# Performance work log

Hardware: AMD Instinct MI355X
Metric: run time of the kernel (lower is better)

Reference implementation:

```python
import jax, jax.numpy as jnp
from jax import lax
import numpy as np

HIDDEN = 1024
GRID = 512
KSIZE = 3
SIGMA = 1.0


def setup_inputs() -> dict:
    key = jax.random.key(0)
    ks = jax.random.split(key, 10)
    B, E, D = 4, 256, 128
    s = 1.0 / np.sqrt(HIDDEN)
    sf = 1.0 / np.sqrt(2 * GRID)
    return {
        "encoder_hidden": jax.random.normal(ks[0], (B, E, HIDDEN), jnp.float32),
        "decoder_hidden": jax.random.normal(ks[1], (B, D, HIDDEN), jnp.float32),
        "encoder_mask": jnp.ones((B, E), jnp.float32),
        "decoder_mask": jnp.ones((B, D), jnp.float32),
        "W_enc": jax.random.uniform(ks[2], (GRID, HIDDEN), jnp.float32, -s, s),
        "b_enc": jax.random.uniform(ks[3], (GRID,), jnp.float32, -s, s),
        "W_dec": jax.random.uniform(ks[4], (GRID, HIDDEN), jnp.float32, -s, s),
        "b_dec": jax.random.uniform(ks[5], (GRID,), jnp.float32, -s, s),
        "W_fus": jax.random.uniform(ks[6], (GRID, 2 * GRID), jnp.float32, -sf, sf),
        "b_fus": jax.random.uniform(ks[7], (GRID,), jnp.float32, -sf, sf),
    }


def _gauss_kernel():
    coords = jnp.arange(KSIZE, dtype=jnp.float32) - KSIZE // 2
    g = jnp.exp(-coords ** 2 / (2.0 * SIGMA ** 2))
    return g / g.sum()


def _blur_axis(x, axis, k):
    # zero-padded 'same' 1D conv with kernel size 3 along `axis`
    pad = [(0, 0)] * x.ndim
    pad[axis] = (1, 1)
    xp = jnp.pad(x, pad)
    n = x.shape[axis]
    return (k[0] * lax.slice_in_dim(xp, 0, n, axis=axis)
            + k[1] * lax.slice_in_dim(xp, 1, n + 1, axis=axis)
            + k[2] * lax.slice_in_dim(xp, 2, n + 2, axis=axis))


def reference(encoder_hidden, decoder_hidden, encoder_mask, decoder_mask,
              W_enc, b_enc, W_dec, b_dec, W_fus, b_fus):
    # projections, masked
    enc_proj = (jnp.einsum('beh,gh->beg', encoder_hidden, W_enc) + b_enc) * encoder_mask[..., None]
    dec_proj = (jnp.einsum('bdh,gh->bdg', decoder_hidden, W_dec) + b_dec) * decoder_mask[..., None]
    # fusion Linear over concat([enc, dec]) == W_fus[:, :G] @ enc + W_fus[:, G:] @ dec + b
    Wf_e = W_fus[:, :GRID]
    Wf_d = W_fus[:, GRID:]
    enc_term = jnp.einsum('beg,og->beo', enc_proj, Wf_e)   # [B,E,G]
    dec_term = jnp.einsum('bdg,og->bdo', dec_proj, Wf_d)   # [B,D,G]
    grid = dec_term[:, :, None, :] + enc_term[:, None, :, :] + b_fus  # [B,D,E,G]
    # separable depthwise Gaussian blur: enc axis (2) then dec axis (1)
    k = _gauss_kernel()
    blurred = _blur_axis(grid, 2, k)
    blurred = _blur_axis(blurred, 1, k)
    # binary mask via L2 norm threshold (threshold=0.0)
    mask = (jnp.linalg.norm(blurred, axis=-1) > 0.0).astype(jnp.float32)
    return (grid, mask)
```

## Files before the change

### kernel.cpp

```cpp
#include <hip/hip_runtime.h>

namespace {

constexpr int kGrid = 512;
constexpr int kB = 4;
constexpr int kE = 256;
constexpr int kD = 128;

constexpr float kG0   = 0.27406862f;
constexpr float kG1   = 0.45186276f;
constexpr float kEdge = kG0 + kG1;

typedef __attribute__((ext_vector_type(8))) short bf16x8;
typedef __attribute__((ext_vector_type(4))) float f32x4;

__device__ __forceinline__ ushort f2bf(float f) {
  union { float f; uint u; } v{f};
  return (ushort)((v.u + 0x7fffu + ((v.u >> 16) & 1u)) >> 16);
}

__global__ __launch_bounds__(256)
void convert_all(const float* __restrict__ enc_h, const float* __restrict__ dec_h,
                 const float* __restrict__ W_fus, ushort* __restrict__ hid,
                 ushort* __restrict__ wfus) {
  const int idx = (blockIdx.x * 256 + threadIdx.x) * 4;
  const float* src; ushort* dst;
  if (idx < 1048576)       { src = enc_h + idx;             dst = hid + idx; }
  else if (idx < 1572864)  { src = dec_h + (idx - 1048576); dst = hid + idx; }
  else                     { src = W_fus + (idx - 1572864); dst = wfus + (idx - 1572864); }
  const float4 v = *(const float4*)src;
  ushort4 o; o.x = f2bf(v.x); o.y = f2bf(v.y); o.z = f2bf(v.z); o.w = f2bf(v.w);
  *(ushort4*)dst = o;
}

__global__ __launch_bounds__(256)
void transpose_cvt(const float* __restrict__ W_enc, const float* __restrict__ W_dec,
                   ushort* __restrict__ WT) {
  const float* Wsrc = blockIdx.z ? W_dec : W_enc;
  ushort* outT = WT + (size_t)blockIdx.z * 1024 * 512;
  __shared__ ushort Ts[32][36];
  const int h0 = blockIdx.x * 32, g0 = blockIdx.y * 32;
  const int tx = threadIdx.x & 7, ty = threadIdx.x >> 3;
  const float4 v = *(const float4*)(Wsrc + (size_t)(g0 + ty) * 1024 + h0 + tx * 4);
  Ts[tx * 4 + 0][ty] = f2bf(v.x); Ts[tx * 4 + 1][ty] = f2bf(v.y);
  Ts[tx * 4 + 2][ty] = f2bf(v.z); Ts[tx * 4 + 3][ty] = f2bf(v.w);
  __syncthreads();
  ushort4 o; o.x = Ts[ty][tx * 4 + 0]; o.y = Ts[ty][tx * 4 + 1];
  o.z = Ts[ty][tx * 4 + 2]; o.w = Ts[ty][tx * 4 + 3];
  *(ushort4*)(outT + (size_t)(h0 + ty) * 512 + g0 + tx * 4) = o;
}

__global__ __launch_bounds__(256)
void cvec_kernel(const float* __restrict__ W_fus, const float* __restrict__ b_enc,
                 const float* __restrict__ b_dec, float* __restrict__ cvec) {
  const int wid = blockIdx.x * 4 + (threadIdx.x >> 6);
  const int lane = threadIdx.x & 63;
  const int sel = wid >> 9, o = wid & 511;
  const float* wrow = W_fus + (size_t)o * 1024 + sel * 512 + lane * 8;
  const float* bv = (sel ? b_dec : b_enc) + lane * 8;
  float s = 0.f;
#pragma unroll
  for (int j = 0; j < 8; ++j) s += wrow[j] * bv[j];
#pragma unroll
  for (int off = 32; off; off >>= 1) s += __shfl_down(s, off);
  if (!lane) cvec[wid] = s;
}


__global__ __launch_bounds__(256)
void gemm_w(const ushort* __restrict__ wfus, const ushort* __restrict__ WT,
            ushort* __restrict__ Mmat) {
  const int z = blockIdx.z;
  const short* A = (const short*)wfus + z * 512;
  const short* B = (const short*)WT + (size_t)z * 1024 * 512;
  ushort* Cw = Mmat + (size_t)z * 512 * 1024;
  __shared__ short As[64][72], Bs[64][72];
  const int tid = threadIdx.x, wid = tid >> 6, lane = tid & 63;
  const int row0 = blockIdx.y * 64, col0 = blockIdx.x * 64;
  const int srow = tid >> 2, sc = tid & 3;
  const short* Ap = A + (size_t)(row0 + srow) * 1024 + sc * 8;
  const short* Bp = B + (size_t)(col0 + srow) * 512 + sc * 8;
  const int wr = (wid >> 1) * 32, wc = (wid & 1) * 32;
  const int r16 = lane & 15, kb = lane >> 4;
  f32x4 acc[2][2] = {};
  for (int k0 = 0; k0 < 512; k0 += 64) {
    const bf16x8 alo = *(const bf16x8*)(Ap + k0);
    const bf16x8 ahi = *(const bf16x8*)(Ap + k0 + 32);
    const bf16x8 blo = *(const bf16x8*)(Bp + k0);
    const bf16x8 bhi = *(const bf16x8*)(Bp + k0 + 32);
    __syncthreads();
    *(bf16x8*)&As[srow][sc * 8] = alo;  *(bf16x8*)&As[srow][(sc + 4) * 8] = ahi;
    *(bf16x8*)&Bs[srow][sc * 8] = blo;  *(bf16x8*)&Bs[srow][(sc + 4) * 8] = bhi;
    __syncthreads();
#pragma unroll
    for (int ks = 0; ks < 2; ++ks) {
      const int ko = ks * 32 + kb * 8;
      const bf16x8 a0 = *(const bf16x8*)&As[wr + r16][ko];
      const bf16x8 a1 = *(const bf16x8*)&As[wr + 16 + r16][ko];
      const bf16x8 b0 = *(const bf16x8*)&Bs[wc + r16][ko];
      const bf16x8 b1 = *(const bf16x8*)&Bs[wc + 16 + r16][ko];
      acc[0][0] = __builtin_amdgcn_mfma_f32_16x16x32_bf16(a0, b0, acc[0][0], 0, 0, 0);
      acc[0][1] = __builtin_amdgcn_mfma_f32_16x16x32_bf16(a0, b1, acc[0][1], 0, 0, 0);
      acc[1][0] = __builtin_amdgcn_mfma_f32_16x16x32_bf16(a1, b0, acc[1][0], 0, 0, 0);
      acc[1][1] = __builtin_amdgcn_mfma_f32_16x16x32_bf16(a1, b1, acc[1][1], 0, 0, 0);
    }
  }
#pragma unroll
  for (int i = 0; i < 2; ++i)
#pragma unroll
    for (int j = 0; j < 2; ++j)
#pragma unroll
      for (int q = 0; q < 4; ++q) {
        const int r = row0 + wr + i * 16 + kb * 4 + q;
        const int c = col0 + wc + j * 16 + r16;
        Cw[(size_t)r * 1024 + c] = f2bf(acc[i][j][q]);
      }
}

__global__ __launch_bounds__(256)
void gemm_t(const ushort* __restrict__ hid, const ushort* __restrict__ Mmat,
            const float* __restrict__ cvec, const float* __restrict__ enc_mask,
            const float* __restrict__ dec_mask, float* __restrict__ term) {
  const int row0 = blockIdx.y * 64, col0 = blockIdx.x * 64;
  const bool enc = row0 < 1024;
  const short* A = (const short*)hid;
  const short* B = (const short*)Mmat + (enc ? 0 : (size_t)512 * 1024);
  const float* cv = cvec + (enc ? 0 : 512);
  const float* rmb = enc ? enc_mask : (dec_mask - 1024);
  __shared__ short As[64][72], Bs[64][72];
  const int tid = threadIdx.x, wid = tid >> 6, lane = tid & 63;
  const int srow = tid >> 2, sc = tid & 3;
  const short* Ap = A + (size_t)(row0 + srow) * 1024 + sc * 8;
  const short* Bp = B + (size_t)(col0 + srow) * 1024 + sc * 8;
  const int wr = (wid >> 1) * 32, wc = (wid & 1) * 32;
  const int r16 = lane & 15, kb = lane >> 4;
  f32x4 acc[2][2] = {};
  for (int k0 = 0; k0 < 1024; k0 += 64) {
    const bf16x8 alo = *(const bf16x8*)(Ap + k0);
    const bf16x8 ahi = *(const bf16x8*)(Ap + k0 + 32);
    const bf16x8 blo = *(const bf16x8*)(Bp + k0);
    const bf16x8 bhi = *(const bf16x8*)(Bp + k0 + 32);
    __syncthreads();
    *(bf16x8*)&As[srow][sc * 8] = alo;  *(bf16x8*)&As[srow][(sc + 4) * 8] = ahi;
    *(bf16x8*)&Bs[srow][sc * 8] = blo;  *(bf16x8*)&Bs[srow][(sc + 4) * 8] = bhi;
    __syncthreads();
#pragma unroll
    for (int ks = 0; ks < 2; ++ks) {
      const int ko = ks * 32 + kb * 8;
      const bf16x8 a0 = *(const bf16x8*)&As[wr + r16][ko];
      const bf16x8 a1 = *(const bf16x8*)&As[wr + 16 + r16][ko];
      const bf16x8 b0 = *(const bf16x8*)&Bs[wc + r16][ko];
      const bf16x8 b1 = *(const bf16x8*)&Bs[wc + 16 + r16][ko];
      acc[0][0] = __builtin_amdgcn_mfma_f32_16x16x32_bf16(a0, b0, acc[0][0], 0, 0, 0);
      acc[0][1] = __builtin_amdgcn_mfma_f32_16x16x32_bf16(a0, b1, acc[0][1], 0, 0, 0);
      acc[1][0] = __builtin_amdgcn_mfma_f32_16x16x32_bf16(a1, b0, acc[1][0], 0, 0, 0);
      acc[1][1] = __builtin_amdgcn_mfma_f32_16x16x32_bf16(a1, b1, acc[1][1], 0, 0, 0);
    }
  }
#pragma unroll
  for (int i = 0; i < 2; ++i)
#pragma unroll
    for (int j = 0; j < 2; ++j)
#pragma unroll
      for (int q = 0; q < 4; ++q) {
        const int r = row0 + wr + i * 16 + kb * 4 + q;
        const int c = col0 + wc + j * 16 + r16;
        term[(size_t)r * 512 + c] = (acc[i][j][q] + cv[c]) * rmb[r];
      }
}

__global__ __launch_bounds__(256)
void assemble(const float* __restrict__ dec_term, const float* __restrict__ enc_term,
              const float* __restrict__ b_fus, float* __restrict__ out) {
  const int bd = blockIdx.x;
  const int b  = bd >> 7;
  const int ebase = blockIdx.y * 64;
  const int tid = threadIdx.x;
  const int eo = tid >> 7;
  const int o4 = (tid & 127) << 2;
  const float4 dv = *(const float4*)(dec_term + (size_t)bd * kGrid + o4);
  const float4 bv = *(const float4*)(b_fus + o4);
  const float4 db = make_float4(dv.x + bv.x, dv.y + bv.y, dv.z + bv.z, dv.w + bv.w);
  const float* encb = enc_term + (size_t)b * kE * kGrid;
  float* outb = out + (size_t)bd * kE * kGrid;
#pragma unroll 4
  for (int e0 = 0; e0 < 64; e0 += 2) {
    const int e = ebase + e0 + eo;
    const float4 ev = *(const float4*)(encb + (size_t)e * kGrid + o4);
    *(float4*)(outb + (size_t)e * kGrid + o4) =
        make_float4(db.x + ev.x, db.y + ev.y, db.z + ev.z, db.w + ev.w);
  }
}

__global__ __launch_bounds__(256)
void blur_both(const float* __restrict__ dec_term, const float* __restrict__ enc_term,
               float* __restrict__ dec_blur, float* __restrict__ enc_blur) {
  const int idx = blockIdx.x * 256 + threadIdx.x;
  constexpr int decN = kB * kD * kGrid;
  if (idx < decN) {
    const int d = (idx >> 9) & (kD - 1);
    float v = kG1 * dec_term[idx];
    if (d > 0)      v += kG0 * dec_term[idx - kGrid];
    if (d < kD - 1) v += kG0 * dec_term[idx + kGrid];
    dec_blur[idx] = v;
  } else {
    const int j = idx - decN;
    if (j < kB * kE * kGrid) {
      const int e = (j >> 9) & (kE - 1);
      float v = kG1 * enc_term[j];
      if (e > 0)      v += kG0 * enc_term[j - kGrid];
      if (e < kE - 1) v += kG0 * enc_term[j + kGrid];
      enc_blur[j] = v;
    }
  }
}

__global__ __launch_bounds__(256)
void mask_kernel(const float* __restrict__ dec_blur, const float* __restrict__ enc_blur,
                 const float* __restrict__ b_fus, float* __restrict__ mask_out) {
  const int bid = blockIdx.x * 4 + (threadIdx.x >> 6);
  const int e = bid & (kE - 1);
  const int d = (bid >> 8) & (kD - 1);
  const int b = bid >> 15;
  const float sE  = (e == 0 || e == kE - 1) ? kEdge : 1.f;
  const float sD  = (d == 0 || d == kD - 1) ? kEdge : 1.f;
  const float sED = sE * sD;
  const int lane = threadIdx.x & 63;
  const float* dp = dec_blur + ((size_t)(b * kD + d)) * kGrid + lane * 8;
  const float* ep = enc_blur + ((size_t)(b * kE + e)) * kGrid + lane * 8;
  const float* zp = b_fus + lane * 8;
  float acc = 0.f;
#pragma unroll
  for (int j = 0; j < 2; ++j) {
    const float4 dv = *(const float4*)(dp + 4 * j);
    const float4 ev = *(const float4*)(ep + 4 * j);
    const float4 zv = *(const float4*)(zp + 4 * j);
    float t;
    t = dv.x * sE + ev.x * sD + zv.x * sED; acc += t * t;
    t = dv.y * sE + ev.y * sD + zv.y * sED; acc += t * t;
    t = dv.z * sE + ev.z * sD + zv.z * sED; acc += t * t;
    t = dv.w * sE + ev.w * sD + zv.w * sED; acc += t * t;
  }
#pragma unroll
  for (int off = 32; off; off >>= 1) acc += __shfl_down(acc, off);
  if (!lane) mask_out[bid] = (acc > 0.f) ? 1.f : 0.f;
}

}

extern "C" void kernel_launch(void* const* d_in, const int* in_sizes, int n_in,
                              void* d_out, int out_size, void* d_ws, size_t ws_size,
                              hipStream_t stream) {
  const float* enc_h  = (const float*)d_in[0];
  const float* dec_h  = (const float*)d_in[1];
  const float* enc_m  = (const float*)d_in[2];
  const float* dec_m  = (const float*)d_in[3];
  const float* W_enc  = (const float*)d_in[4];
  const float* b_enc  = (const float*)d_in[5];
  const float* W_dec  = (const float*)d_in[6];
  const float* b_dec  = (const float*)d_in[7];
  const float* W_fus  = (const float*)d_in[8];
  const float* b_fus  = (const float*)d_in[9];
  float* out = (float*)d_out;
  float* ws  = (float*)d_ws;

  float* term = ws;
  float* cvec = ws + 786432;
  ushort* hid  = (ushort*)(ws + 787456);
  ushort* wfus = hid + 1572864;
  ushort* WT   = wfus + 524288;
  ushort* Mmat = WT + 1048576;
  float* enc_term = term;
  float* dec_term = term + 524288;
  float* dec_blur = (float*)hid;
  float* enc_blur = dec_blur + 262144;

  const dim3 blk(256);
  hipLaunchKernelGGL(convert_all, dim3(2048), blk, 0, stream, enc_h, dec_h, W_fus, hid, wfus);
  hipLaunchKernelGGL(transpose_cvt, dim3(32, 16, 2), blk, 0, stream, W_enc, W_dec, WT);
  hipLaunchKernelGGL(cvec_kernel, dim3(256), blk, 0, stream, W_fus, b_enc, b_dec, cvec);
  hipLaunchKernelGGL(gemm_w, dim3(16, 8, 2), blk, 0, stream, wfus, WT, Mmat);
  hipLaunchKernelGGL(gemm_t, dim3(8, 24), blk, 0, stream, hid, Mmat, cvec, enc_m, dec_m, term);
  hipLaunchKernelGGL(assemble, dim3(kB * kD, kE / 64), blk, 0, stream,
                     dec_term, enc_term, b_fus, out);
  hipLaunchKernelGGL(blur_both, dim3(3072), blk, 0, stream,
                     dec_term, enc_term, dec_blur, enc_blur);
  hipLaunchKernelGGL(mask_kernel, dim3(kB * kD * kE / 4), blk, 0, stream,
                     dec_blur, enc_blur, b_fus, out + (size_t)kB * kD * kE * kGrid);
}
```

Measured before the change: 385.5 us.

## Fuse whole pipeline into one persistent cooperative kernel with grid syncs

Replaces the eight separate kernels with a single cooperative kernel that runs the projection GEMM, the fusion GEMM, the blur, the grid assembly and the mask in phases separated by grid-wide syncs. fp32 inputs are converted to bf16 while being staged into shared memory, which removes the separate conversion and transpose passes. The precomputed combined weight matrix is dropped in favour of computing the projections first and then the fusion GEMM. This cuts launch overhead and intermediate traffic, at the cost of grid synchronisation and of GEMM phases that use only a fraction of the resident blocks.

```diff
diff --git a/kernel.cpp b/kernel.cpp
--- a/kernel.cpp
+++ b/kernel.cpp
@@ -1,11 +1,9 @@
 #include <hip/hip_runtime.h>
+#include <hip/hip_cooperative_groups.h>
+
+namespace cg = cooperative_groups;
 
 namespace {
-
-constexpr int kGrid = 512;
-constexpr int kB = 4;
-constexpr int kE = 256;
-constexpr int kD = 128;
 
 constexpr float kG0   = 0.27406862f;
 constexpr float kG1   = 0.45186276f;
@@ -19,231 +17,208 @@
   return (ushort)((v.u + 0x7fffu + ((v.u >> 16) & 1u)) >> 16);
 }
 
-__global__ __launch_bounds__(256)
-void convert_all(const float* __restrict__ enc_h, const float* __restrict__ dec_h,
-                 const float* __restrict__ W_fus, ushort* __restrict__ hid,
-                 ushort* __restrict__ wfus) {
-  const int idx = (blockIdx.x * 256 + threadIdx.x) * 4;
-  const float* src; ushort* dst;
-  if (idx < 1048576)       { src = enc_h + idx;             dst = hid + idx; }
-  else if (idx < 1572864)  { src = dec_h + (idx - 1048576); dst = hid + idx; }
-  else                     { src = W_fus + (idx - 1572864); dst = wfus + (idx - 1572864); }
-  const float4 v = *(const float4*)src;
-  ushort4 o; o.x = f2bf(v.x); o.y = f2bf(v.y); o.z = f2bf(v.z); o.w = f2bf(v.w);
-  *(ushort4*)dst = o;
-}
-
-__global__ __launch_bounds__(256)
-void transpose_cvt(const float* __restrict__ W_enc, const float* __restrict__ W_dec,
-                   ushort* __restrict__ WT) {
-  const float* Wsrc = blockIdx.z ? W_dec : W_enc;
-  ushort* outT = WT + (size_t)blockIdx.z * 1024 * 512;
-  __shared__ ushort Ts[32][36];
-  const int h0 = blockIdx.x * 32, g0 = blockIdx.y * 32;
-  const int tx = threadIdx.x & 7, ty = threadIdx.x >> 3;
-  const float4 v = *(const float4*)(Wsrc + (size_t)(g0 + ty) * 1024 + h0 + tx * 4);
-  Ts[tx * 4 + 0][ty] = f2bf(v.x); Ts[tx * 4 + 1][ty] = f2bf(v.y);
-  Ts[tx * 4 + 2][ty] = f2bf(v.z); Ts[tx * 4 + 3][ty] = f2bf(v.w);
-  __syncthreads();
-  ushort4 o; o.x = Ts[ty][tx * 4 + 0]; o.y = Ts[ty][tx * 4 + 1];
-  o.z = Ts[ty][tx * 4 + 2]; o.w = Ts[ty][tx * 4 + 3];
-  *(ushort4*)(outT + (size_t)(h0 + ty) * 512 + g0 + tx * 4) = o;
-}
-
-__global__ __launch_bounds__(256)
-void cvec_kernel(const float* __restrict__ W_fus, const float* __restrict__ b_enc,
-                 const float* __restrict__ b_dec, float* __restrict__ cvec) {
-  const int wid = blockIdx.x * 4 + (threadIdx.x >> 6);
-  const int lane = threadIdx.x & 63;
-  const int sel = wid >> 9, o = wid & 511;
-  const float* wrow = W_fus + (size_t)o * 1024 + sel * 512 + lane * 8;
-  const float* bv = (sel ? b_dec : b_enc) + lane * 8;
-  float s = 0.f;
-#pragma unroll
-  for (int j = 0; j < 8; ++j) s += wrow[j] * bv[j];
-#pragma unroll
-  for (int off = 32; off; off >>= 1) s += __shfl_down(s, off);
-  if (!lane) cvec[wid] = s;
-}
-
-
-__global__ __launch_bounds__(256)
-void gemm_w(const ushort* __restrict__ wfus, const ushort* __restrict__ WT,
-            ushort* __restrict__ Mmat) {
-  const int z = blockIdx.z;
-  const short* A = (const short*)wfus + z * 512;
-  const short* B = (const short*)WT + (size_t)z * 1024 * 512;
-  ushort* Cw = Mmat + (size_t)z * 512 * 1024;
+__device__ __forceinline__ void cvt_store16(const float4 v0, const float4 v1,
+                                            const float4 v2, const float4 v3,
+                                            short* dst) {
+  bf16x8 lo, hi;
+  lo[0] = (short)f2bf(v0.x); lo[1] = (short)f2bf(v0.y);
+  lo[2] = (short)f2bf(v0.z); lo[3] = (short)f2bf(v0.w);
+  lo[4] = (short)f2bf(v1.x); lo[5] = (short)f2bf(v1.y);
+  lo[6] = (short)f2bf(v1.z); lo[7] = (short)f2bf(v1.w);
+  hi[0] = (short)f2bf(v2.x); hi[1] = (short)f2bf(v2.y);
+  hi[2] = (short)f2bf(v2.z); hi[3] = (short)f2bf(v2.w);
+  hi[4] = (short)f2bf(v3.x); hi[5] = (short)f2bf(v3.y);
+  hi[6] = (short)f2bf(v3.z); hi[7] = (short)f2bf(v3.w);
+  *(bf16x8*)dst = lo;
+  *(bf16x8*)(dst + 8) = hi;
+}
+
+__global__ __launch_bounds__(256, 3)
+void fused(const float* __restrict__ enc_h, const float* __restrict__ dec_h,
+           const float* __restrict__ enc_m, const float* __restrict__ dec_m,
+           const float* __restrict__ W_enc, const float* __restrict__ b_enc,
+           const float* __restrict__ W_dec, const float* __restrict__ b_dec,
+           const float* __restrict__ W_fus, const float* __restrict__ b_fus,
+           float* __restrict__ out, ushort* __restrict__ proj,
+           float* __restrict__ term, float* __restrict__ dec_blur,
+           float* __restrict__ enc_blur) {
+  cg::grid_group grid = cg::this_grid();
   __shared__ short As[64][72], Bs[64][72];
-  const int tid = threadIdx.x, wid = tid >> 6, lane = tid & 63;
-  const int row0 = blockIdx.y * 64, col0 = blockIdx.x * 64;
+  const int tid = threadIdx.x;
+  const int wid = tid >> 6, lane = tid & 63;
   const int srow = tid >> 2, sc = tid & 3;
-  const short* Ap = A + (size_t)(row0 + srow) * 1024 + sc * 8;
-  const short* Bp = B + (size_t)(col0 + srow) * 512 + sc * 8;
   const int wr = (wid >> 1) * 32, wc = (wid & 1) * 32;
   const int r16 = lane & 15, kb = lane >> 4;
-  f32x4 acc[2][2] = {};
-  for (int k0 = 0; k0 < 512; k0 += 64) {
-    const bf16x8 alo = *(const bf16x8*)(Ap + k0);
-    const bf16x8 ahi = *(const bf16x8*)(Ap + k0 + 32);
-    const bf16x8 blo = *(const bf16x8*)(Bp + k0);
-    const bf16x8 bhi = *(const bf16x8*)(Bp + k0 + 32);
-    __syncthreads();
-    *(bf16x8*)&As[srow][sc * 8] = alo;  *(bf16x8*)&As[srow][(sc + 4) * 8] = ahi;
-    *(bf16x8*)&Bs[srow][sc * 8] = blo;  *(bf16x8*)&Bs[srow][(sc + 4) * 8] = bhi;
-    __syncthreads();
-#pragma unroll
-    for (int ks = 0; ks < 2; ++ks) {
-      const int ko = ks * 32 + kb * 8;
-      const bf16x8 a0 = *(const bf16x8*)&As[wr + r16][ko];
-      const bf16x8 a1 = *(const bf16x8*)&As[wr + 16 + r16][ko];
-      const bf16x8 b0 = *(const bf16x8*)&Bs[wc + r16][ko];
-      const bf16x8 b1 = *(const bf16x8*)&Bs[wc + 16 + r16][ko];
-      acc[0][0] = __builtin_amdgcn_mfma_f32_16x16x32_bf16(a0, b0, acc[0][0], 0, 0, 0);
-      acc[0][1] = __builtin_amdgcn_mfma_f32_16x16x32_bf16(a0, b1, acc[0][1], 0, 0, 0);
-      acc[1][0] = __builtin_amdgcn_mfma_f32_16x16x32_bf16(a1, b0, acc[1][0], 0, 0, 0);
-      acc[1][1] = __builtin_amdgcn_mfma_f32_16x16x32_bf16(a1, b1, acc[1][1], 0, 0, 0);
-    }
-  }
-#pragma unroll
-  for (int i = 0; i < 2; ++i)
-#pragma unroll
-    for (int j = 0; j < 2; ++j)
-#pragma unroll
-      for (int q = 0; q < 4; ++q) {
-        const int r = row0 + wr + i * 16 + kb * 4 + q;
-        const int c = col0 + wc + j * 16 + r16;
-        Cw[(size_t)r * 1024 + c] = f2bf(acc[i][j][q]);
-      }
-}
-
-__global__ __launch_bounds__(256)
-void gemm_t(const ushort* __restrict__ hid, const ushort* __restrict__ Mmat,
-            const float* __restrict__ cvec, const float* __restrict__ enc_mask,
-            const float* __restrict__ dec_mask, float* __restrict__ term) {
-  const int row0 = blockIdx.y * 64, col0 = blockIdx.x * 64;
-  const bool enc = row0 < 1024;
-  const short* A = (const short*)hid;
-  const short* B = (const short*)Mmat + (enc ? 0 : (size_t)512 * 1024);
-  const float* cv = cvec + (enc ? 0 : 512);
-  const float* rmb = enc ? enc_mask : (dec_mask - 1024);
-  __shared__ short As[64][72], Bs[64][72];
-  const int tid = threadIdx.x, wid = tid >> 6, lane = tid & 63;
-  const int srow = tid >> 2, sc = tid & 3;
-  const short* Ap = A + (size_t)(row0 + srow) * 1024 + sc * 8;
-  const short* Bp = B + (size_t)(col0 + srow) * 1024 + sc * 8;
-  const int wr = (wid >> 1) * 32, wc = (wid & 1) * 32;
-  const int r16 = lane & 15, kb = lane >> 4;
-  f32x4 acc[2][2] = {};
-  for (int k0 = 0; k0 < 1024; k0 += 64) {
-    const bf16x8 alo = *(const bf16x8*)(Ap + k0);
-    const bf16x8 ahi = *(const bf16x8*)(Ap + k0 + 32);
-    const bf16x8 blo = *(const bf16x8*)(Bp + k0);
-    const bf16x8 bhi = *(const bf16x8*)(Bp + k0 + 32);
-    __syncthreads();
-    *(bf16x8*)&As[srow][sc * 8] = alo;  *(bf16x8*)&As[srow][(sc + 4) * 8] = ahi;
-    *(bf16x8*)&Bs[srow][sc * 8] = blo;  *(bf16x8*)&Bs[srow][(sc + 4) * 8] = bhi;
-    __syncthreads();
-#pragma unroll
-    for (int ks = 0; ks < 2; ++ks) {
-      const int ko = ks * 32 + kb * 8;
-      const bf16x8 a0 = *(const bf16x8*)&As[wr + r16][ko];
-      const bf16x8 a1 = *(const bf16x8*)&As[wr + 16 + r16][ko];
-      const bf16x8 b0 = *(const bf16x8*)&Bs[wc + r16][ko];
-      const bf16x8 b1 = *(const bf16x8*)&Bs[wc + 16 + r16][ko];
-      acc[0][0] = __builtin_amdgcn_mfma_f32_16x16x32_bf16(a0, b0, acc[0][0], 0, 0, 0);
-      acc[0][1] = __builtin_amdgcn_mfma_f32_16x16x32_bf16(a0, b1, acc[0][1], 0, 0, 0);
-      acc[1][0] = __builtin_amdgcn_mfma_f32_16x16x32_bf16(a1, b0, acc[1][0], 0, 0, 0);
-      acc[1][1] = __builtin_amdgcn_mfma_f32_16x16x32_bf16(a1, b1, acc[1][1], 0, 0, 0);
-    }
-  }
-#pragma unroll
-  for (int i = 0; i < 2; ++i)
-#pragma unroll
-    for (int j = 0; j < 2; ++j)
-#pragma unroll
-      for (int q = 0; q < 4; ++q) {
-        const int r = row0 + wr + i * 16 + kb * 4 + q;
-        const int c = col0 + wc + j * 16 + r16;
-        term[(size_t)r * 512 + c] = (acc[i][j][q] + cv[c]) * rmb[r];
-      }
-}
-
-__global__ __launch_bounds__(256)
-void assemble(const float* __restrict__ dec_term, const float* __restrict__ enc_term,
-              const float* __restrict__ b_fus, float* __restrict__ out) {
-  const int bd = blockIdx.x;
-  const int b  = bd >> 7;
-  const int ebase = blockIdx.y * 64;
-  const int tid = threadIdx.x;
-  const int eo = tid >> 7;
-  const int o4 = (tid & 127) << 2;
-  const float4 dv = *(const float4*)(dec_term + (size_t)bd * kGrid + o4);
-  const float4 bv = *(const float4*)(b_fus + o4);
-  const float4 db = make_float4(dv.x + bv.x, dv.y + bv.y, dv.z + bv.z, dv.w + bv.w);
-  const float* encb = enc_term + (size_t)b * kE * kGrid;
-  float* outb = out + (size_t)bd * kE * kGrid;
+
+  for (int t = blockIdx.x; t < 192; t += gridDim.x) {
+    const int row0 = (t >> 3) * 64, col0 = (t & 7) * 64;
+    const bool enc = row0 < 1024;
+    const float* Ap = (enc ? enc_h + (size_t)row0 * 1024
+                           : dec_h + (size_t)(row0 - 1024) * 1024)
+                      + (size_t)srow * 1024 + sc * 16;
+    const float* Bp = (enc ? W_enc : W_dec)
+                      + (size_t)(col0 + srow) * 1024 + sc * 16;
+    f32x4 acc[2][2] = {};
+    for (int k0 = 0; k0 < 1024; k0 += 64) {
+      const float4 a0 = *(const float4*)(Ap + k0);
+      const float4 a1 = *(const float4*)(Ap + k0 + 4);
+      const float4 a2 = *(const float4*)(Ap + k0 + 8);
+      const float4 a3 = *(const float4*)(Ap + k0 + 12);
+      const float4 b0 = *(const float4*)(Bp + k0);
+      const float4 b1 = *(const float4*)(Bp + k0 + 4);
+      const float4 b2 = *(const float4*)(Bp + k0 + 8);
+      const float4 b3 = *(const float4*)(Bp + k0 + 12);
+      __syncthreads();
+      cvt_store16(a0, a1, a2, a3, &As[srow][sc * 16]);
+      cvt_store16(b0, b1, b2, b3, &Bs[srow][sc * 16]);
+      __syncthreads();
+#pragma unroll
+      for (int ks = 0; ks < 2; ++ks) {
+        const int ko = ks * 32 + kb * 8;
+        const bf16x8 fa0 = *(const bf16x8*)&As[wr + r16][ko];
+        const bf16x8 fa1 = *(const bf16x8*)&As[wr + 16 + r16][ko];
+        const bf16x8 fb0 = *(const bf16x8*)&Bs[wc + r16][ko];
+        const bf16x8 fb1 = *(const bf16x8*)&Bs[wc + 16 + r16][ko];
+        acc[0][0] = __builtin_amdgcn_mfma_f32_16x16x32_bf16(fa0, fb0, acc[0][0], 0, 0, 0);
+        acc[0][1] = __builtin_amdgcn_mfma_f32_16x16x32_bf16(fa0, fb1, acc[0][1], 0, 0, 0);
+        acc[1][0] = __builtin_amdgcn_mfma_f32_16x16x32_bf16(fa1, fb0, acc[1][0], 0, 0, 0);
+        acc[1][1] = __builtin_amdgcn_mfma_f32_16x16x32_bf16(fa1, fb1, acc[1][1], 0, 0, 0);
+      }
+    }
+    const float* bias = enc ? b_enc : b_dec;
+    const float* rm   = enc ? enc_m : (dec_m - 1024);
+#pragma unroll
+    for (int i = 0; i < 2; ++i)
+#pragma unroll
+      for (int j = 0; j < 2; ++j)
+#pragma unroll
+        for (int q = 0; q < 4; ++q) {
+          const int r = row0 + wr + i * 16 + kb * 4 + q;
+          const int c = col0 + wc + j * 16 + r16;
+          proj[(size_t)r * 512 + c] = f2bf((acc[i][j][q] + bias[c]) * rm[r]);
+        }
+  }
+  grid.sync();
+
+  for (int t = blockIdx.x; t < 192; t += gridDim.x) {
+    const int row0 = (t >> 3) * 64, col0 = (t & 7) * 64;
+    const bool enc = row0 < 1024;
+    const short* Ap = (const short*)proj + (size_t)(row0 + srow) * 512 + sc * 16;
+    const float* Bp = W_fus + (size_t)(col0 + srow) * 1024 + (enc ? 0 : 512) + sc * 16;
+    f32x4 acc[2][2] = {};
+    for (int k0 = 0; k0 < 512; k0 += 64) {
+      const bf16x8 alo = *(const bf16x8*)(Ap + k0);
+      const bf16x8 ahi = *(const bf16x8*)(Ap + k0 + 8);
+      const float4 b0 = *(const float4*)(Bp + k0);
+      const float4 b1 = *(const float4*)(Bp + k0 + 4);
+      const float4 b2 = *(const float4*)(Bp + k0 + 8);
+      const float4 b3 = *(const float4*)(Bp + k0 + 12);
+      __syncthreads();
+      *(bf16x8*)&As[srow][sc * 16] = alo;
+      *(bf16x8*)&As[srow][sc * 16 + 8] = ahi;
+      cvt_store16(b0, b1, b2, b3, &Bs[srow][sc * 16]);
+      __syncthreads();
+#pragma unroll
+      for (int ks = 0; ks < 2; ++ks) {
+        const int ko = ks * 32 + kb * 8;
+        const bf16x8 fa0 = *(const bf16x8*)&As[wr + r16][ko];
+        const bf16x8 fa1 = *(const bf16x8*)&As[wr + 16 + r16][ko];
+        const bf16x8 fb0 = *(const bf16x8*)&Bs[wc + r16][ko];
+        const bf16x8 fb1 = *(const bf16x8*)&Bs[wc + 16 + r16][ko];
+        acc[0][0] = __builtin_amdgcn_mfma_f32_16x16x32_bf16(fa0, fb0, acc[0][0], 0, 0, 0);
+        acc[0][1] = __builtin_amdgcn_mfma_f32_16x16x32_bf16(fa0, fb1, acc[0][1], 0, 0, 0);
+        acc[1][0] = __builtin_amdgcn_mfma_f32_16x16x32_bf16(fa1, fb0, acc[1][0], 0, 0, 0);
+        acc[1][1] = __builtin_amdgcn_mfma_f32_16x16x32_bf16(fa1, fb1, acc[1][1], 0, 0, 0);
+      }
+    }
+#pragma unroll
+    for (int i = 0; i < 2; ++i)
+#pragma unroll
+      for (int j = 0; j < 2; ++j)
+#pragma unroll
+        for (int q = 0; q < 4; ++q) {
+          const int r = row0 + wr + i * 16 + kb * 4 + q;
+          const int c = col0 + wc + j * 16 + r16;
+          term[(size_t)r * 512 + c] = acc[i][j][q];
+        }
+  }
+  grid.sync();
+
+  {
+    const float* dterm = term + 524288;
+    for (int blk = blockIdx.x; blk < 3072; blk += gridDim.x) {
+      const int idx = blk * 256 + tid;
+      if (idx < 262144) {
+        const int d = (idx >> 9) & 127;
+        float v = kG1 * dterm[idx];
+        if (d > 0)   v += kG0 * dterm[idx - 512];
+        if (d < 127) v += kG0 * dterm[idx + 512];
+        dec_blur[idx] = v;
+      } else {
+        const int j = idx - 262144;
+        const int e = (j >> 9) & 255;
+        float v = kG1 * term[j];
+        if (e > 0)   v += kG0 * term[j - 512];
+        if (e < 255) v += kG0 * term[j + 512];
+        enc_blur[j] = v;
+      }
+    }
+  }
+  grid.sync();
+
+  {
+    const float* dterm = term + 524288;
+    const int eo = tid >> 7;
+    const int o4 = (tid & 127) << 2;
+    for (int u = blockIdx.x; u < 2048; u += gridDim.x) {
+      const int bd = u >> 2;
+      const int b = bd >> 7;
+      const int ebase = (u & 3) * 64;
+      const float4 dv = *(const float4*)(dterm + (size_t)bd * 512 + o4);
+      const float4 bv = *(const float4*)(b_fus + o4);
+      const float4 db = make_float4(dv.x + bv.x, dv.y + bv.y, dv.z + bv.z, dv.w + bv.w);
+      const float* encb = term + (size_t)b * 256 * 512;
+      float* outb = out + (size_t)bd * 256 * 512;
 #pragma unroll 4
-  for (int e0 = 0; e0 < 64; e0 += 2) {
-    const int e = ebase + e0 + eo;
-    const float4 ev = *(const float4*)(encb + (size_t)e * kGrid + o4);
-    *(float4*)(outb + (size_t)e * kGrid + o4) =
-        make_float4(db.x + ev.x, db.y + ev.y, db.z + ev.z, db.w + ev.w);
-  }
-}
-
-__global__ __launch_bounds__(256)
-void blur_both(const float* __restrict__ dec_term, const float* __restrict__ enc_term,
-               float* __restrict__ dec_blur, float* __restrict__ enc_blur) {
-  const int idx = blockIdx.x * 256 + threadIdx.x;
-  constexpr int decN = kB * kD * kGrid;
-  if (idx < decN) {
-    const int d = (idx >> 9) & (kD - 1);
-    float v = kG1 * dec_term[idx];
-    if (d > 0)      v += kG0 * dec_term[idx - kGrid];
-    if (d < kD - 1) v += kG0 * dec_term[idx + kGrid];
-    dec_blur[idx] = v;
-  } else {
-    const int j = idx - decN;
-    if (j < kB * kE * kGrid) {
-      const int e = (j >> 9) & (kE - 1);
-      float v = kG1 * enc_term[j];
-      if (e > 0)      v += kG0 * enc_term[j - kGrid];
-      if (e < kE - 1) v += kG0 * enc_term[j + kGrid];
-      enc_blur[j] = v;
-    }
-  }
-}
-
-__global__ __launch_bounds__(256)
-void mask_kernel(const float* __restrict__ dec_blur, const float* __restrict__ enc_blur,
-                 const float* __restrict__ b_fus, float* __restrict__ mask_out) {
-  const int bid = blockIdx.x * 4 + (threadIdx.x >> 6);
-  const int e = bid & (kE - 1);
-  const int d = (bid >> 8) & (kD - 1);
-  const int b = bid >> 15;
-  const float sE  = (e == 0 || e == kE - 1) ? kEdge : 1.f;
-  const float sD  = (d == 0 || d == kD - 1) ? kEdge : 1.f;
-  const float sED = sE * sD;
-  const int lane = threadIdx.x & 63;
-  const float* dp = dec_blur + ((size_t)(b * kD + d)) * kGrid + lane * 8;
-  const float* ep = enc_blur + ((size_t)(b * kE + e)) * kGrid + lane * 8;
-  const float* zp = b_fus + lane * 8;
-  float acc = 0.f;
-#pragma unroll
-  for (int j = 0; j < 2; ++j) {
-    const float4 dv = *(const float4*)(dp + 4 * j);
-    const float4 ev = *(const float4*)(ep + 4 * j);
-    const float4 zv = *(const float4*)(zp + 4 * j);
-    float t;
-    t = dv.x * sE + ev.x * sD + zv.x * sED; acc += t * t;
-    t = dv.y * sE + ev.y * sD + zv.y * sED; acc += t * t;
-    t = dv.z * sE + ev.z * sD + zv.z * sED; acc += t * t;
-    t = dv.w * sE + ev.w * sD + zv.w * sED; acc += t * t;
-  }
-#pragma unroll
-  for (int off = 32; off; off >>= 1) acc += __shfl_down(acc, off);
-  if (!lane) mask_out[bid] = (acc > 0.f) ? 1.f : 0.f;
+      for (int e0 = 0; e0 < 64; e0 += 2) {
+        const int e = ebase + e0 + eo;
+        const float4 ev = *(const float4*)(encb + (size_t)e * 512 + o4);
+        *(float4*)(outb + (size_t)e * 512 + o4) =
+            make_float4(db.x + ev.x, db.y + ev.y, db.z + ev.z, db.w + ev.w);
+      }
+    }
+  }
+
+  {
+    float* mask_out = out + (size_t)4 * 128 * 256 * 512;
+    for (int g = blockIdx.x; g < 32768; g += gridDim.x) {
+      const int bid = g * 4 + wid;
+      const int e = bid & 255;
+      const int d = (bid >> 8) & 127;
+      const int b = bid >> 15;
+      const float sE  = (e == 0 || e == 255) ? kEdge : 1.f;
+      const float sD  = (d == 0 || d == 127) ? kEdge : 1.f;
+      const float sED = sE * sD;
+      const float* dp = dec_blur + ((size_t)(b * 128 + d)) * 512 + lane * 8;
+      const float* ep = enc_blur + ((size_t)(b * 256 + e)) * 512 + lane * 8;
+      const float* zp = b_fus + lane * 8;
+      float acc = 0.f;
+#pragma unroll
+      for (int j = 0; j < 2; ++j) {
+        const float4 dv = *(const float4*)(dp + 4 * j);
+        const float4 ev = *(const float4*)(ep + 4 * j);
+        const float4 zv = *(const float4*)(zp + 4 * j);
+        float tt;
+        tt = dv.x * sE + ev.x * sD + zv.x * sED; acc += tt * tt;
+        tt = dv.y * sE + ev.y * sD + zv.y * sED; acc += tt * tt;
+        tt = dv.z * sE + ev.z * sD + zv.z * sED; acc += tt * tt;
+        tt = dv.w * sE + ev.w * sD + zv.w * sED; acc += tt * tt;
+      }
+#pragma unroll
+      for (int off = 32; off; off >>= 1) acc += __shfl_down(acc, off);
+      if (!lane) mask_out[bid] = (acc > 0.f) ? 1.f : 0.f;
+    }
+  }
 }
 
 }
@@ -251,40 +226,40 @@
 extern "C" void kernel_launch(void* const* d_in, const int* in_sizes, int n_in,
                               void* d_out, int out_size, void* d_ws, size_t ws_size,
                               hipStream_t stream) {
-  const float* enc_h  = (const float*)d_in[0];
-  const float* dec_h  = (const float*)d_in[1];
-  const float* enc_m  = (const float*)d_in[2];
-  const float* dec_m  = (const float*)d_in[3];
-  const float* W_enc  = (const float*)d_in[4];
-  const float* b_enc  = (const float*)d_in[5];
-  const float* W_dec  = (const float*)d_in[6];
-  const float* b_dec  = (const float*)d_in[7];
-  const float* W_fus  = (const float*)d_in[8];
-  const float* b_fus  = (const float*)d_in[9];
+  const float* enc_h = (const float*)d_in[0];
+  const float* dec_h = (const float*)d_in[1];
+  const float* enc_m = (const float*)d_in[2];
+  const float* dec_m = (const float*)d_in[3];
+  const float* W_enc = (const float*)d_in[4];
+  const float* b_enc = (const float*)d_in[5];
+  const float* W_dec = (const float*)d_in[6];
+  const float* b_dec = (const float*)d_in[7];
+  const float* W_fus = (const float*)d_in[8];
+  const float* b_fus = (const float*)d_in[9];
   float* out = (float*)d_out;
   float* ws  = (float*)d_ws;
 
-  float* term = ws;
-  float* cvec = ws + 786432;
-  ushort* hid  = (ushort*)(ws + 787456);
-  ushort* wfus = hid + 1572864;
-  ushort* WT   = wfus + 524288;
-  ushort* Mmat = WT + 1048576;
-  float* enc_term = term;
-  float* dec_term = term + 524288;
-  float* dec_blur = (float*)hid;
-  float* enc_blur = dec_blur + 262144;
-
-  const dim3 blk(256);
-  hipLaunchKernelGGL(convert_all, dim3(2048), blk, 0, stream, enc_h, dec_h, W_fus, hid, wfus);
-  hipLaunchKernelGGL(transpose_cvt, dim3(32, 16, 2), blk, 0, stream, W_enc, W_dec, WT);
-  hipLaunchKernelGGL(cvec_kernel, dim3(256), blk, 0, stream, W_fus, b_enc, b_dec, cvec);
-  hipLaunchKernelGGL(gemm_w, dim3(16, 8, 2), blk, 0, stream, wfus, WT, Mmat);
-  hipLaunchKernelGGL(gemm_t, dim3(8, 24), blk, 0, stream, hid, Mmat, cvec, enc_m, dec_m, term);
-  hipLaunchKernelGGL(assemble, dim3(kB * kD, kE / 64), blk, 0, stream,
-                     dec_term, enc_term, b_fus, out);
-  hipLaunchKernelGGL(blur_both, dim3(3072), blk, 0, stream,
-                     dec_term, enc_term, dec_blur, enc_blur);
-  hipLaunchKernelGGL(mask_kernel, dim3(kB * kD * kE / 4), blk, 0, stream,
-                     dec_blur, enc_blur, b_fus, out + (size_t)kB * kD * kE * kGrid);
-}
+  float*  term     = ws;
+  ushort* proj     = (ushort*)(ws + 786432);
+  float*  dec_blur = ws + 786432 + 393216;
+  float*  enc_blur = dec_blur + 262144;
+
+  int dev = 0;
+  (void)hipGetDevice(&dev);
+  int cus = 256;
+  (void)hipDeviceGetAttribute(&cus, hipDeviceAttributeMultiprocessorCount, dev);
+  if (cus <= 0) cus = 256;
+  int maxb = 3;
+  (void)hipOccupancyMaxActiveBlocksPerMultiprocessor(&maxb, (const void*)fused, 256, 0);
+  if (maxb < 1) maxb = 1;
+  long nb = (long)cus * (long)maxb;
+  if (nb > 2048) nb = 2048;
+  if (nb < 8) nb = 8;
+
+  void* args[] = {(void*)&enc_h, (void*)&dec_h, (void*)&enc_m, (void*)&dec_m,
+                  (void*)&W_enc, (void*)&b_enc, (void*)&W_dec, (void*)&b_dec,
+                  (void*)&W_fus, (void*)&b_fus, (void*)&out, (void*)&proj,
+                  (void*)&term, (void*)&dec_blur, (void*)&enc_blur};
+  (void)hipLaunchCooperativeKernel((const void*)fused, dim3((unsigned)nb), dim3(256),
+                                   args, 0, stream);
+}
```

New measurement: 651.2 us. 68.9% more time.
